# Kernel optimization log

Measured on AMD Instinct MI355X. Metric: run time of the kernel, lower is better.

Reference implementation:

```python
import math
import jax, jax.numpy as jnp
import numpy as np

B, CH3, T = 64, 192, 2048  # B = batch*heads, CH3 = 3*head_dim

def setup_inputs() -> dict:
    key = jax.random.key(0)
    qkv = jax.random.normal(key, (B, CH3, T), dtype=jnp.float32)
    return {"qkv": qkv}

def reference(qkv):
    ch = qkv.shape[1] // 3
    q, k, v = jnp.split(qkv, 3, axis=1)  # each [B, ch, T]
    scale = 1.0 / math.sqrt(math.sqrt(ch))
    # scores [B, T(query), S(key)]
    weight = jnp.einsum('bct,bcs->bts', q * scale, k * scale)
    weight = jax.nn.softmax(weight.astype(jnp.float32), axis=-1).astype(weight.dtype)
    return jnp.einsum('bts,bcs->bct', weight, v)
```

## Files before the change

### kernel.cpp

```cpp
#include <hip/hip_runtime.h>


#define DHEAD 64
#define TLEN  2048
#define NB    64
#define BQ    256
#define BK    64
#define NT    (TLEN / BK)
#define LDT   65

typedef _Float16 h16x8 __attribute__((ext_vector_type(8)));
typedef _Float16 h16x2 __attribute__((ext_vector_type(2)));
typedef __fp16   fp16x2 __attribute__((ext_vector_type(2)));
typedef float    f32x16 __attribute__((ext_vector_type(16)));

#define QK_SCALE 0.42466090267246895f

extern "C" __device__ float __ocml_native_exp2_f32(float);

union H2U  { h16x2 h; fp16x2 f; unsigned u; };
union FRAG { h16x8 v; unsigned u[4]; };

__device__ __forceinline__ unsigned pk_u(float a, float b) {
    H2U x; x.f = __builtin_amdgcn_cvt_pkrtz(a, b); return x.u;
}

__device__ __forceinline__ int swz(int row, int col) {
    return row * 64 + (col ^ ((row & 7) << 3));
}

__global__ __launch_bounds__(256)
void prep_k(const float* __restrict__ qkv, _Float16* __restrict__ ws) {
    __shared__ float T32[64 * LDT];
    const int tile = blockIdx.x, b = blockIdx.y;
    const int tid = threadIdx.x;
    const float* src = qkv + ((size_t)b * 3 + 1) * DHEAD * TLEN + tile * 64;
    _Float16* dst = ws + (size_t)b * DHEAD * TLEN + (size_t)tile * 64 * DHEAD;
    {
        int c = tid >> 4, t4 = (tid & 15) * 4;
        #pragma unroll
        for (int rr = 0; rr < 4; ++rr, c += 16) {
            float4 f = *(const float4*)(src + c * TLEN + t4);
            T32[(t4 + 0) * LDT + c] = f.x;
            T32[(t4 + 1) * LDT + c] = f.y;
            T32[(t4 + 2) * LDT + c] = f.z;
            T32[(t4 + 3) * LDT + c] = f.w;
        }
    }
    __syncthreads();
    #pragma unroll
    for (int rep = 0; rep < 2; ++rep) {
        int idx = rep * 256 + tid;
        int t = idx >> 3, j = idx & 7;
        const float* row = &T32[t * LDT + j * 8];
        FRAG o;
        o.u[0] = pk_u(row[0] * QK_SCALE, row[1] * QK_SCALE);
        o.u[1] = pk_u(row[2] * QK_SCALE, row[3] * QK_SCALE);
        o.u[2] = pk_u(row[4] * QK_SCALE, row[5] * QK_SCALE);
        o.u[3] = pk_u(row[6] * QK_SCALE, row[7] * QK_SCALE);
        *(h16x8*)(dst + t * DHEAD + j * 8) = o.v;
    }
}

__global__ __launch_bounds__(256, 2)
void attn(const float* __restrict__ qkv, const _Float16* __restrict__ kt,
          float* __restrict__ out) {
    __shared__ alignas(16) _Float16 Ks[64 * 64];
    __shared__ alignas(16) _Float16 Vs[64 * 64];

    const int tid  = threadIdx.x;
    const int wave = tid >> 6;
    const int lane = tid & 63;
    const int h    = lane >> 5;
    const int c32  = lane & 31;

    const int flat = blockIdx.x + (int)gridDim.x * blockIdx.y;
    const int j8   = flat & 7, m8 = flat >> 3;
    const int b    = ((m8 & 7) << 3) | j8;
    const int t0   = (m8 >> 3) * BQ + wave * 64;

    const float* qg = qkv + ((size_t)b * 3 + 0) * DHEAD * TLEN;
    const float* vg = qkv + ((size_t)b * 3 + 2) * DHEAD * TLEN;
    const _Float16* kb = kt + (size_t)b * DHEAD * TLEN;

    h16x8 qf[2][4];
    #pragma unroll
    for (int nb = 0; nb < 2; ++nb)
        #pragma unroll
        for (int kbq = 0; kbq < 4; ++kbq) {
            const float* qp = qg + (size_t)(kbq * 16 + h * 8) * TLEN + t0 + nb * 32 + c32;
            FRAG f;
            #pragma unroll
            for (int w = 0; w < 4; ++w)
                f.u[w] = pk_u(qp[(size_t)(2 * w) * TLEN] * QK_SCALE,
                              qp[(size_t)(2 * w + 1) * TLEN] * QK_SCALE);
            qf[nb][kbq] = f.v;
        }

    f32x16 acco[2][2];
    #pragma unroll
    for (int cb = 0; cb < 2; ++cb)
        #pragma unroll
        for (int nb = 0; nb < 2; ++nb)
            #pragma unroll
            for (int r = 0; r < 16; ++r) acco[cb][nb][r] = 0.f;
    float lp[2] = {0.f, 0.f};

    const int sr = tid >> 2;
    const int sq = (tid & 3) * 16;

    h16x8 kc2[2], vc2[2];

    auto PREF = [&](int s0) {
        const _Float16* kp = kb + (size_t)(s0 + sr) * DHEAD + sq;
        kc2[0] = *(const h16x8*)(kp);
        kc2[1] = *(const h16x8*)(kp + 8);
        const float* vp = vg + (size_t)sr * TLEN + s0 + sq;
        float4 v0 = *(const float4*)(vp + 0);
        float4 v1 = *(const float4*)(vp + 4);
        float4 v2 = *(const float4*)(vp + 8);
        float4 v3 = *(const float4*)(vp + 12);
        FRAG a, c;
        a.u[0] = pk_u(v0.x, v0.y); a.u[1] = pk_u(v0.z, v0.w);
        a.u[2] = pk_u(v1.x, v1.y); a.u[3] = pk_u(v1.z, v1.w);
        c.u[0] = pk_u(v2.x, v2.y); c.u[1] = pk_u(v2.z, v2.w);
        c.u[2] = pk_u(v3.x, v3.y); c.u[3] = pk_u(v3.z, v3.w);
        vc2[0] = a.v; vc2[1] = c.v;
    };

    PREF(0);

    for (int it = 0; it < NT; ++it) {
        __syncthreads();
        *(h16x8*)&Ks[swz(sr, sq)]     = kc2[0];
        *(h16x8*)&Ks[swz(sr, sq + 8)] = kc2[1];
        *(h16x8*)&Vs[swz(sr, sq)]     = vc2[0];
        *(h16x8*)&Vs[swz(sr, sq + 8)] = vc2[1];
        __syncthreads();

        if (it + 1 < NT) PREF((it + 1) * BK);

        #pragma unroll
        for (int mb = 0; mb < 2; ++mb) {
            f32x16 accs[2];
            #pragma unroll
            for (int nb = 0; nb < 2; ++nb)
                #pragma unroll
                for (int r = 0; r < 16; ++r) accs[nb][r] = 0.f;

            __builtin_amdgcn_s_setprio(1);
            #pragma unroll
            for (int kbq = 0; kbq < 4; ++kbq) {
                h16x8 ka = *(const h16x8*)&Ks[swz(mb * 32 + c32, kbq * 16 + h * 8)];
                accs[0] = __builtin_amdgcn_mfma_f32_32x32x16_f16(ka, qf[0][kbq], accs[0], 0, 0, 0);
                accs[1] = __builtin_amdgcn_mfma_f32_32x32x16_f16(ka, qf[1][kbq], accs[1], 0, 0, 0);
            }
            __builtin_amdgcn_s_setprio(0);

            h16x8 pb[2][2];
            #pragma unroll
            for (int nb = 0; nb < 2; ++nb) {
                float e[16];
                #pragma unroll
                for (int r = 0; r < 16; ++r) e[r] = __ocml_native_exp2_f32(accs[nb][r]);
                float s0 = 0.f;
                #pragma unroll
                for (int r = 0; r < 16; ++r) s0 += e[r];
                lp[nb] += s0;
                #pragma unroll
                for (int kb16 = 0; kb16 < 2; ++kb16) {
                    const float* ee = e + kb16 * 8;
                    unsigned a01 = pk_u(ee[0], ee[1]);
                    unsigned a23 = pk_u(ee[2], ee[3]);
                    unsigned b01 = pk_u(ee[4], ee[5]);
                    unsigned b23 = pk_u(ee[6], ee[7]);
                    asm volatile("v_permlane32_swap_b32 %0, %1" : "+v"(a01), "+v"(b01));
                    asm volatile("v_permlane32_swap_b32 %0, %1" : "+v"(a23), "+v"(b23));
                    FRAG f;
                    f.u[0] = a01; f.u[1] = a23; f.u[2] = b01; f.u[3] = b23;
                    pb[kb16][nb] = f.v;
                }
            }

            __builtin_amdgcn_s_setprio(1);
            #pragma unroll
            for (int kb16 = 0; kb16 < 2; ++kb16) {
                const int scol = mb * 32 + kb16 * 16 + h * 8;
                #pragma unroll
                for (int cb = 0; cb < 2; ++cb) {
                    h16x8 va = *(const h16x8*)&Vs[swz(cb * 32 + c32, scol)];
                    acco[cb][0] = __builtin_amdgcn_mfma_f32_32x32x16_f16(va, pb[kb16][0], acco[cb][0], 0, 0, 0);
                    acco[cb][1] = __builtin_amdgcn_mfma_f32_32x32x16_f16(va, pb[kb16][1], acco[cb][1], 0, 0, 0);
                }
            }
            __builtin_amdgcn_s_setprio(0);
        }
    }

    float rinv[2];
    #pragma unroll
    for (int nb = 0; nb < 2; ++nb) {
        float l = lp[nb];
        l += __shfl_xor(l, 32);
        rinv[nb] = 1.0f / l;
    }

    float* ob = out + (size_t)b * DHEAD * TLEN + t0;
    #pragma unroll
    for (int cb = 0; cb < 2; ++cb)
        #pragma unroll
        for (int nb = 0; nb < 2; ++nb)
            #pragma unroll
            for (int r = 0; r < 16; ++r) {
                const int c = cb * 32 + (r & 3) + 8 * (r >> 2) + 4 * h;
                ob[(size_t)c * TLEN + nb * 32 + c32] = acco[cb][nb][r] * rinv[nb];
            }
}

extern "C" void kernel_launch(void* const* d_in, const int* in_sizes, int n_in,
                              void* d_out, int out_size, void* d_ws, size_t ws_size,
                              hipStream_t stream) {
    const float* qkv = (const float*)d_in[0];
    _Float16* ws = (_Float16*)d_ws;
    float* out = (float*)d_out;
    prep_k<<<dim3(TLEN / 64, NB), 256, 0, stream>>>(qkv, ws);
    attn<<<dim3(TLEN / BQ, NB), 256, 0, stream>>>(qkv, ws, out);
}
```

Measured before the change: 219.9 us.

## Halve query tile per wave, double-buffer K/V LDS, raise occupancy

Each wave now handles 32 queries instead of 64, so the per-block query tile drops to 128 and the grid doubles. Accumulator and Q-fragment registers are halved, and launch bounds now ask for 4 blocks per CU. K/V shared tiles are double-buffered, which removes one barrier per iteration. The cost is that each K/V tile is reused by half as many queries, doubling global and LDS traffic for K/V per unit of work, and the block-to-(batch, tile) mapping is reworked.

```diff
diff --git a/kernel.cpp b/kernel.cpp
--- a/kernel.cpp
+++ b/kernel.cpp
@@ -4,7 +4,7 @@
 #define DHEAD 64
 #define TLEN  2048
 #define NB    64
-#define BQ    256
+#define BQ    128
 #define BK    64
 #define NT    (TLEN / BK)
 #define LDT   65
@@ -62,11 +62,11 @@
     }
 }
 
-__global__ __launch_bounds__(256, 2)
+__global__ __launch_bounds__(256, 4)
 void attn(const float* __restrict__ qkv, const _Float16* __restrict__ kt,
           float* __restrict__ out) {
-    __shared__ alignas(16) _Float16 Ks[64 * 64];
-    __shared__ alignas(16) _Float16 Vs[64 * 64];
+    __shared__ alignas(16) _Float16 Ks[2][64 * 64];
+    __shared__ alignas(16) _Float16 Vs[2][64 * 64];
 
     const int tid  = threadIdx.x;
     const int wave = tid >> 6;
@@ -75,36 +75,31 @@
     const int c32  = lane & 31;
 
     const int flat = blockIdx.x + (int)gridDim.x * blockIdx.y;
-    const int j8   = flat & 7, m8 = flat >> 3;
-    const int b    = ((m8 & 7) << 3) | j8;
-    const int t0   = (m8 >> 3) * BQ + wave * 64;
+    const int b    = (((flat >> 7) & 7) << 3) | (flat & 7);
+    const int t0   = ((flat >> 3) & 15) * BQ + wave * 32;
 
     const float* qg = qkv + ((size_t)b * 3 + 0) * DHEAD * TLEN;
     const float* vg = qkv + ((size_t)b * 3 + 2) * DHEAD * TLEN;
     const _Float16* kb = kt + (size_t)b * DHEAD * TLEN;
 
-    h16x8 qf[2][4];
-    #pragma unroll
-    for (int nb = 0; nb < 2; ++nb)
-        #pragma unroll
-        for (int kbq = 0; kbq < 4; ++kbq) {
-            const float* qp = qg + (size_t)(kbq * 16 + h * 8) * TLEN + t0 + nb * 32 + c32;
-            FRAG f;
-            #pragma unroll
-            for (int w = 0; w < 4; ++w)
-                f.u[w] = pk_u(qp[(size_t)(2 * w) * TLEN] * QK_SCALE,
-                              qp[(size_t)(2 * w + 1) * TLEN] * QK_SCALE);
-            qf[nb][kbq] = f.v;
-        }
-
-    f32x16 acco[2][2];
+    h16x8 qf[4];
+    #pragma unroll
+    for (int kbq = 0; kbq < 4; ++kbq) {
+        const float* qp = qg + (size_t)(kbq * 16 + h * 8) * TLEN + t0 + c32;
+        FRAG f;
+        #pragma unroll
+        for (int w = 0; w < 4; ++w)
+            f.u[w] = pk_u(qp[(size_t)(2 * w) * TLEN] * QK_SCALE,
+                          qp[(size_t)(2 * w + 1) * TLEN] * QK_SCALE);
+        qf[kbq] = f.v;
+    }
+
+    f32x16 acco[2];
     #pragma unroll
     for (int cb = 0; cb < 2; ++cb)
         #pragma unroll
-        for (int nb = 0; nb < 2; ++nb)
-            #pragma unroll
-            for (int r = 0; r < 16; ++r) acco[cb][nb][r] = 0.f;
-    float lp[2] = {0.f, 0.f};
+        for (int r = 0; r < 16; ++r) acco[cb][r] = 0.f;
+    float lp = 0.f;
 
     const int sr = tid >> 2;
     const int sq = (tid & 3) * 16;
@@ -131,55 +126,51 @@
     PREF(0);
 
     for (int it = 0; it < NT; ++it) {
+        _Float16* ksb = Ks[it & 1];
+        _Float16* vsb = Vs[it & 1];
+        *(h16x8*)&ksb[swz(sr, sq)]     = kc2[0];
+        *(h16x8*)&ksb[swz(sr, sq + 8)] = kc2[1];
+        *(h16x8*)&vsb[swz(sr, sq)]     = vc2[0];
+        *(h16x8*)&vsb[swz(sr, sq + 8)] = vc2[1];
         __syncthreads();
-        *(h16x8*)&Ks[swz(sr, sq)]     = kc2[0];
-        *(h16x8*)&Ks[swz(sr, sq + 8)] = kc2[1];
-        *(h16x8*)&Vs[swz(sr, sq)]     = vc2[0];
-        *(h16x8*)&Vs[swz(sr, sq + 8)] = vc2[1];
-        __syncthreads();
 
         if (it + 1 < NT) PREF((it + 1) * BK);
 
         #pragma unroll
         for (int mb = 0; mb < 2; ++mb) {
-            f32x16 accs[2];
-            #pragma unroll
-            for (int nb = 0; nb < 2; ++nb)
-                #pragma unroll
-                for (int r = 0; r < 16; ++r) accs[nb][r] = 0.f;
+            f32x16 accs;
+            #pragma unroll
+            for (int r = 0; r < 16; ++r) accs[r] = 0.f;
 
             __builtin_amdgcn_s_setprio(1);
             #pragma unroll
             for (int kbq = 0; kbq < 4; ++kbq) {
-                h16x8 ka = *(const h16x8*)&Ks[swz(mb * 32 + c32, kbq * 16 + h * 8)];
-                accs[0] = __builtin_amdgcn_mfma_f32_32x32x16_f16(ka, qf[0][kbq], accs[0], 0, 0, 0);
-                accs[1] = __builtin_amdgcn_mfma_f32_32x32x16_f16(ka, qf[1][kbq], accs[1], 0, 0, 0);
+                h16x8 ka = *(const h16x8*)&ksb[swz(mb * 32 + c32, kbq * 16 + h * 8)];
+                accs = __builtin_amdgcn_mfma_f32_32x32x16_f16(ka, qf[kbq], accs, 0, 0, 0);
             }
             __builtin_amdgcn_s_setprio(0);
 
-            h16x8 pb[2][2];
-            #pragma unroll
-            for (int nb = 0; nb < 2; ++nb) {
-                float e[16];
-                #pragma unroll
-                for (int r = 0; r < 16; ++r) e[r] = __ocml_native_exp2_f32(accs[nb][r]);
-                float s0 = 0.f;
-                #pragma unroll
-                for (int r = 0; r < 16; ++r) s0 += e[r];
-                lp[nb] += s0;
-                #pragma unroll
-                for (int kb16 = 0; kb16 < 2; ++kb16) {
-                    const float* ee = e + kb16 * 8;
-                    unsigned a01 = pk_u(ee[0], ee[1]);
-                    unsigned a23 = pk_u(ee[2], ee[3]);
-                    unsigned b01 = pk_u(ee[4], ee[5]);
-                    unsigned b23 = pk_u(ee[6], ee[7]);
-                    asm volatile("v_permlane32_swap_b32 %0, %1" : "+v"(a01), "+v"(b01));
-                    asm volatile("v_permlane32_swap_b32 %0, %1" : "+v"(a23), "+v"(b23));
-                    FRAG f;
-                    f.u[0] = a01; f.u[1] = a23; f.u[2] = b01; f.u[3] = b23;
-                    pb[kb16][nb] = f.v;
-                }
+            float e[16];
+            #pragma unroll
+            for (int r = 0; r < 16; ++r) e[r] = __ocml_native_exp2_f32(accs[r]);
+            float s0 = 0.f;
+            #pragma unroll
+            for (int r = 0; r < 16; ++r) s0 += e[r];
+            lp += s0;
+
+            h16x8 pb[2];
+            #pragma unroll
+            for (int kb16 = 0; kb16 < 2; ++kb16) {
+                const float* ee = e + kb16 * 8;
+                unsigned a01 = pk_u(ee[0], ee[1]);
+                unsigned a23 = pk_u(ee[2], ee[3]);
+                unsigned b01 = pk_u(ee[4], ee[5]);
+                unsigned b23 = pk_u(ee[6], ee[7]);
+                asm volatile("v_permlane32_swap_b32 %0, %1" : "+v"(a01), "+v"(b01));
+                asm volatile("v_permlane32_swap_b32 %0, %1" : "+v"(a23), "+v"(b23));
+                FRAG f;
+                f.u[0] = a01; f.u[1] = a23; f.u[2] = b01; f.u[3] = b23;
+                pb[kb16] = f.v;
             }
 
             __builtin_amdgcn_s_setprio(1);
@@ -188,33 +179,26 @@
                 const int scol = mb * 32 + kb16 * 16 + h * 8;
                 #pragma unroll
                 for (int cb = 0; cb < 2; ++cb) {
-                    h16x8 va = *(const h16x8*)&Vs[swz(cb * 32 + c32, scol)];
-                    acco[cb][0] = __builtin_amdgcn_mfma_f32_32x32x16_f16(va, pb[kb16][0], acco[cb][0], 0, 0, 0);
-                    acco[cb][1] = __builtin_amdgcn_mfma_f32_32x32x16_f16(va, pb[kb16][1], acco[cb][1], 0, 0, 0);
+                    h16x8 va = *(const h16x8*)&vsb[swz(cb * 32 + c32, scol)];
+                    acco[cb] = __builtin_amdgcn_mfma_f32_32x32x16_f16(va, pb[kb16], acco[cb], 0, 0, 0);
                 }
             }
             __builtin_amdgcn_s_setprio(0);
         }
     }
 
-    float rinv[2];
-    #pragma unroll
-    for (int nb = 0; nb < 2; ++nb) {
-        float l = lp[nb];
-        l += __shfl_xor(l, 32);
-        rinv[nb] = 1.0f / l;
-    }
+    float l = lp;
+    l += __shfl_xor(l, 32);
+    const float rinv = 1.0f / l;
 
     float* ob = out + (size_t)b * DHEAD * TLEN + t0;
     #pragma unroll
     for (int cb = 0; cb < 2; ++cb)
         #pragma unroll
-        for (int nb = 0; nb < 2; ++nb)
-            #pragma unroll
-            for (int r = 0; r < 16; ++r) {
-                const int c = cb * 32 + (r & 3) + 8 * (r >> 2) + 4 * h;
-                ob[(size_t)c * TLEN + nb * 32 + c32] = acco[cb][nb][r] * rinv[nb];
-            }
+        for (int r = 0; r < 16; ++r) {
+            const int c = cb * 32 + (r & 3) + 8 * (r >> 2) + 4 * h;
+            ob[(size_t)c * TLEN + c32] = acco[cb][r] * rinv;
+        }
 }
 
 extern "C" void kernel_launch(void* const* d_in, const int* in_sizes, int n_in,
```

Measured after the change: 228.8 us. +4.1%, slower.

## Split key range across two blocks and add combine kernel

Applied to the files above, without the earlier changes.

Each query tile is now processed by two blocks, each covering half of the key sequence. The grid doubles to 1024 blocks and occupancy is raised to 4 blocks per CU. K fragments are read straight from global memory into registers instead of being staged in LDS. V uses a double-buffered LDS tile with a new layout, which needs only one barrier per iteration. Unnormalised partial outputs and row sums go to workspace, and a third kernel merges and normalises them. This adds extra global traffic and a kernel launch in exchange for more parallelism and less synchronisation.

```diff
diff --git a/kernel.cpp b/kernel.cpp
--- a/kernel.cpp
+++ b/kernel.cpp
@@ -6,8 +6,12 @@
 #define NB    64
 #define BQ    256
 #define BK    64
-#define NT    (TLEN / BK)
+#define HALF_S 1024
+#define NT2   (HALF_S / BK)
 #define LDT   65
+
+#define KT_BYTES (NB * DHEAD * TLEN * 2)
+#define L_BYTES  (2 * NB * TLEN * 4)
 
 typedef _Float16 h16x8 __attribute__((ext_vector_type(8)));
 typedef _Float16 h16x2 __attribute__((ext_vector_type(2)));
@@ -25,8 +29,8 @@
     H2U x; x.f = __builtin_amdgcn_cvt_pkrtz(a, b); return x.u;
 }
 
-__device__ __forceinline__ int swz(int row, int col) {
-    return row * 64 + (col ^ ((row & 7) << 3));
+__device__ __forceinline__ int vidx(int c, int s) {
+    return ((s >> 3) << 9) + (c << 3) + (s & 7);
 }
 
 __global__ __launch_bounds__(256)
@@ -62,11 +66,11 @@
     }
 }
 
-__global__ __launch_bounds__(256, 2)
+__global__ __launch_bounds__(256, 4)
 void attn(const float* __restrict__ qkv, const _Float16* __restrict__ kt,
+          float* __restrict__ lbuf, float* __restrict__ o1,
           float* __restrict__ out) {
-    __shared__ alignas(16) _Float16 Ks[64 * 64];
-    __shared__ alignas(16) _Float16 Vs[64 * 64];
+    __shared__ alignas(16) _Float16 Vs[2][64 * 64];
 
     const int tid  = threadIdx.x;
     const int wave = tid >> 6;
@@ -74,14 +78,18 @@
     const int h    = lane >> 5;
     const int c32  = lane & 31;
 
-    const int flat = blockIdx.x + (int)gridDim.x * blockIdx.y;
-    const int j8   = flat & 7, m8 = flat >> 3;
-    const int b    = ((m8 & 7) << 3) | j8;
-    const int t0   = (m8 >> 3) * BQ + wave * 64;
+    const int flat  = blockIdx.x;
+    const int x     = flat & 7, y = flat >> 3;
+    const int b     = ((y >> 4) << 3) | x;
+    const int inner = y & 15;
+    const int shalf = inner & 1;
+    const int qt    = inner >> 1;
+    const int t0    = qt * BQ + wave * 64;
+    const int sbase = shalf * HALF_S;
 
     const float* qg = qkv + ((size_t)b * 3 + 0) * DHEAD * TLEN;
     const float* vg = qkv + ((size_t)b * 3 + 2) * DHEAD * TLEN;
-    const _Float16* kb = kt + (size_t)b * DHEAD * TLEN;
+    const _Float16* kbp = kt + (size_t)b * DHEAD * TLEN + (size_t)sbase * DHEAD;
 
     h16x8 qf[2][4];
     #pragma unroll
@@ -109,13 +117,9 @@
     const int sr = tid >> 2;
     const int sq = (tid & 3) * 16;
 
-    h16x8 kc2[2], vc2[2];
-
+    h16x8 vc2[2];
     auto PREF = [&](int s0) {
-        const _Float16* kp = kb + (size_t)(s0 + sr) * DHEAD + sq;
-        kc2[0] = *(const h16x8*)(kp);
-        kc2[1] = *(const h16x8*)(kp + 8);
-        const float* vp = vg + (size_t)sr * TLEN + s0 + sq;
+        const float* vp = vg + (size_t)sr * TLEN + sbase + s0 + sq;
         float4 v0 = *(const float4*)(vp + 0);
         float4 v1 = *(const float4*)(vp + 4);
         float4 v2 = *(const float4*)(vp + 8);
@@ -130,15 +134,23 @@
 
     PREF(0);
 
-    for (int it = 0; it < NT; ++it) {
+    for (int it = 0; it < NT2; ++it) {
+        const int s0 = it * BK;
+
+        h16x8 kf[8];
+        #pragma unroll
+        for (int mb = 0; mb < 2; ++mb)
+            #pragma unroll
+            for (int kbq = 0; kbq < 4; ++kbq)
+                kf[mb * 4 + kbq] = *(const h16x8*)(kbp + (size_t)(s0 + mb * 32 + c32) * DHEAD
+                                                   + kbq * 16 + h * 8);
+
+        _Float16* vsb = Vs[it & 1];
+        *(h16x8*)&vsb[vidx(sr, sq)]     = vc2[0];
+        *(h16x8*)&vsb[vidx(sr, sq + 8)] = vc2[1];
         __syncthreads();
-        *(h16x8*)&Ks[swz(sr, sq)]     = kc2[0];
-        *(h16x8*)&Ks[swz(sr, sq + 8)] = kc2[1];
-        *(h16x8*)&Vs[swz(sr, sq)]     = vc2[0];
-        *(h16x8*)&Vs[swz(sr, sq + 8)] = vc2[1];
-        __syncthreads();
-
-        if (it + 1 < NT) PREF((it + 1) * BK);
+
+        if (it + 1 < NT2) PREF((it + 1) * BK);
 
         #pragma unroll
         for (int mb = 0; mb < 2; ++mb) {
@@ -151,7 +163,7 @@
             __builtin_amdgcn_s_setprio(1);
             #pragma unroll
             for (int kbq = 0; kbq < 4; ++kbq) {
-                h16x8 ka = *(const h16x8*)&Ks[swz(mb * 32 + c32, kbq * 16 + h * 8)];
+                h16x8 ka = kf[mb * 4 + kbq];
                 accs[0] = __builtin_amdgcn_mfma_f32_32x32x16_f16(ka, qf[0][kbq], accs[0], 0, 0, 0);
                 accs[1] = __builtin_amdgcn_mfma_f32_32x32x16_f16(ka, qf[1][kbq], accs[1], 0, 0, 0);
             }
@@ -163,10 +175,10 @@
                 float e[16];
                 #pragma unroll
                 for (int r = 0; r < 16; ++r) e[r] = __ocml_native_exp2_f32(accs[nb][r]);
-                float s0 = 0.f;
-                #pragma unroll
-                for (int r = 0; r < 16; ++r) s0 += e[r];
-                lp[nb] += s0;
+                float s0v = 0.f;
+                #pragma unroll
+                for (int r = 0; r < 16; ++r) s0v += e[r];
+                lp[nb] += s0v;
                 #pragma unroll
                 for (int kb16 = 0; kb16 < 2; ++kb16) {
                     const float* ee = e + kb16 * 8;
@@ -188,7 +200,7 @@
                 const int scol = mb * 32 + kb16 * 16 + h * 8;
                 #pragma unroll
                 for (int cb = 0; cb < 2; ++cb) {
-                    h16x8 va = *(const h16x8*)&Vs[swz(cb * 32 + c32, scol)];
+                    h16x8 va = *(const h16x8*)&vsb[vidx(cb * 32 + c32, scol)];
                     acco[cb][0] = __builtin_amdgcn_mfma_f32_32x32x16_f16(va, pb[kb16][0], acco[cb][0], 0, 0, 0);
                     acco[cb][1] = __builtin_amdgcn_mfma_f32_32x32x16_f16(va, pb[kb16][1], acco[cb][1], 0, 0, 0);
                 }
@@ -197,15 +209,15 @@
         }
     }
 
-    float rinv[2];
+    float lsum[2];
     #pragma unroll
     for (int nb = 0; nb < 2; ++nb) {
         float l = lp[nb];
         l += __shfl_xor(l, 32);
-        rinv[nb] = 1.0f / l;
-    }
-
-    float* ob = out + (size_t)b * DHEAD * TLEN + t0;
+        lsum[nb] = l;
+    }
+
+    float* op = (shalf == 0 ? out : o1) + (size_t)b * DHEAD * TLEN + t0;
     #pragma unroll
     for (int cb = 0; cb < 2; ++cb)
         #pragma unroll
@@ -213,16 +225,38 @@
             #pragma unroll
             for (int r = 0; r < 16; ++r) {
                 const int c = cb * 32 + (r & 3) + 8 * (r >> 2) + 4 * h;
-                ob[(size_t)c * TLEN + nb * 32 + c32] = acco[cb][nb][r] * rinv[nb];
-            }
+                op[(size_t)c * TLEN + nb * 32 + c32] = acco[cb][nb][r];
+            }
+    lbuf[(size_t)shalf * NB * TLEN + (size_t)b * TLEN + t0 + lane] = lsum[lane >> 5];
+}
+
+__global__ __launch_bounds__(256)
+void combine(float* __restrict__ out, const float* __restrict__ o1,
+             const float* __restrict__ lbuf) {
+    const size_t i = ((size_t)blockIdx.x * 256 + threadIdx.x) * 4;
+    const int b = (int)(i >> 17);
+    const int t = (int)(i & 2047);
+    float4 a  = *(const float4*)(out + i);
+    float4 c  = *(const float4*)(o1 + i);
+    float4 l0 = *(const float4*)(lbuf + (size_t)b * TLEN + t);
+    float4 l1 = *(const float4*)(lbuf + (size_t)NB * TLEN + (size_t)b * TLEN + t);
+    float4 r;
+    r.x = (a.x + c.x) / (l0.x + l1.x);
+    r.y = (a.y + c.y) / (l0.y + l1.y);
+    r.z = (a.z + c.z) / (l0.z + l1.z);
+    r.w = (a.w + c.w) / (l0.w + l1.w);
+    *(float4*)(out + i) = r;
 }
 
 extern "C" void kernel_launch(void* const* d_in, const int* in_sizes, int n_in,
                               void* d_out, int out_size, void* d_ws, size_t ws_size,
                               hipStream_t stream) {
     const float* qkv = (const float*)d_in[0];
-    _Float16* ws = (_Float16*)d_ws;
     float* out = (float*)d_out;
-    prep_k<<<dim3(TLEN / 64, NB), 256, 0, stream>>>(qkv, ws);
-    attn<<<dim3(TLEN / BQ, NB), 256, 0, stream>>>(qkv, ws, out);
-}
+    _Float16* kt = (_Float16*)d_ws;
+    float* lbuf  = (float*)((char*)d_ws + KT_BYTES);
+    float* o1    = (float*)((char*)d_ws + KT_BYTES + L_BYTES);
+    prep_k<<<dim3(TLEN / 64, NB), 256, 0, stream>>>(qkv, kt);
+    attn<<<dim3(1024), 256, 0, stream>>>(qkv, kt, lbuf, o1, out);
+    combine<<<dim3(NB * DHEAD * TLEN / 1024), 256, 0, stream>>>(out, o1, lbuf);
+}
```

Measured after the change: 445.5 us. 2.03x slower.

## Double-buffer K/V LDS tiles and batch both score blocks before softmax

Applied to the files above, without the earlier changes.

Shared K and V tiles are double-buffered so each iteration needs one barrier instead of two. Within an iteration, both QK^T score blocks are computed first and LDS fragments for K and V are loaded up front, giving the scheduler more independent MFMA and exp work to interleave. The cost is doubled LDS use and more live accumulator registers, which could cause spills or lower occupancy.

```diff
diff --git a/kernel.cpp b/kernel.cpp
--- a/kernel.cpp
+++ b/kernel.cpp
@@ -65,8 +65,8 @@
 __global__ __launch_bounds__(256, 2)
 void attn(const float* __restrict__ qkv, const _Float16* __restrict__ kt,
           float* __restrict__ out) {
-    __shared__ alignas(16) _Float16 Ks[64 * 64];
-    __shared__ alignas(16) _Float16 Vs[64 * 64];
+    __shared__ alignas(16) _Float16 Ks[2][64 * 64];
+    __shared__ alignas(16) _Float16 Vs[2][64 * 64];
 
     const int tid  = threadIdx.x;
     const int wave = tid >> 6;
@@ -131,42 +131,60 @@
     PREF(0);
 
     for (int it = 0; it < NT; ++it) {
+        _Float16* ksb = Ks[it & 1];
+        _Float16* vsb = Vs[it & 1];
+        *(h16x8*)&ksb[swz(sr, sq)]     = kc2[0];
+        *(h16x8*)&ksb[swz(sr, sq + 8)] = kc2[1];
+        *(h16x8*)&vsb[swz(sr, sq)]     = vc2[0];
+        *(h16x8*)&vsb[swz(sr, sq + 8)] = vc2[1];
         __syncthreads();
-        *(h16x8*)&Ks[swz(sr, sq)]     = kc2[0];
-        *(h16x8*)&Ks[swz(sr, sq + 8)] = kc2[1];
-        *(h16x8*)&Vs[swz(sr, sq)]     = vc2[0];
-        *(h16x8*)&Vs[swz(sr, sq + 8)] = vc2[1];
-        __syncthreads();
 
         if (it + 1 < NT) PREF((it + 1) * BK);
 
+        f32x16 accs[2][2];
+        #pragma unroll
+        for (int mb = 0; mb < 2; ++mb)
+            #pragma unroll
+            for (int nb = 0; nb < 2; ++nb)
+                #pragma unroll
+                for (int r = 0; r < 16; ++r) accs[mb][nb][r] = 0.f;
+
         #pragma unroll
         for (int mb = 0; mb < 2; ++mb) {
-            f32x16 accs[2];
-            #pragma unroll
-            for (int nb = 0; nb < 2; ++nb)
-                #pragma unroll
-                for (int r = 0; r < 16; ++r) accs[nb][r] = 0.f;
-
+            h16x8 ka[4];
+            #pragma unroll
+            for (int kbq = 0; kbq < 4; ++kbq)
+                ka[kbq] = *(const h16x8*)&ksb[swz(mb * 32 + c32, kbq * 16 + h * 8)];
             __builtin_amdgcn_s_setprio(1);
             #pragma unroll
             for (int kbq = 0; kbq < 4; ++kbq) {
-                h16x8 ka = *(const h16x8*)&Ks[swz(mb * 32 + c32, kbq * 16 + h * 8)];
-                accs[0] = __builtin_amdgcn_mfma_f32_32x32x16_f16(ka, qf[0][kbq], accs[0], 0, 0, 0);
-                accs[1] = __builtin_amdgcn_mfma_f32_32x32x16_f16(ka, qf[1][kbq], accs[1], 0, 0, 0);
+                accs[mb][0] = __builtin_amdgcn_mfma_f32_32x32x16_f16(ka[kbq], qf[0][kbq], accs[mb][0], 0, 0, 0);
+                accs[mb][1] = __builtin_amdgcn_mfma_f32_32x32x16_f16(ka[kbq], qf[1][kbq], accs[mb][1], 0, 0, 0);
             }
             __builtin_amdgcn_s_setprio(0);
+        }
+
+        #pragma unroll
+        for (int mb = 0; mb < 2; ++mb) {
+            h16x8 va[2][2];
+            #pragma unroll
+            for (int kb16 = 0; kb16 < 2; ++kb16) {
+                const int scol = mb * 32 + kb16 * 16 + h * 8;
+                #pragma unroll
+                for (int cb = 0; cb < 2; ++cb)
+                    va[kb16][cb] = *(const h16x8*)&vsb[swz(cb * 32 + c32, scol)];
+            }
 
             h16x8 pb[2][2];
             #pragma unroll
             for (int nb = 0; nb < 2; ++nb) {
                 float e[16];
                 #pragma unroll
-                for (int r = 0; r < 16; ++r) e[r] = __ocml_native_exp2_f32(accs[nb][r]);
-                float s0 = 0.f;
-                #pragma unroll
-                for (int r = 0; r < 16; ++r) s0 += e[r];
-                lp[nb] += s0;
+                for (int r = 0; r < 16; ++r) e[r] = __ocml_native_exp2_f32(accs[mb][nb][r]);
+                float s0v = 0.f;
+                #pragma unroll
+                for (int r = 0; r < 16; ++r) s0v += e[r];
+                lp[nb] += s0v;
                 #pragma unroll
                 for (int kb16 = 0; kb16 < 2; ++kb16) {
                     const float* ee = e + kb16 * 8;
@@ -184,15 +202,12 @@
 
             __builtin_amdgcn_s_setprio(1);
             #pragma unroll
-            for (int kb16 = 0; kb16 < 2; ++kb16) {
-                const int scol = mb * 32 + kb16 * 16 + h * 8;
+            for (int kb16 = 0; kb16 < 2; ++kb16)
                 #pragma unroll
                 for (int cb = 0; cb < 2; ++cb) {
-                    h16x8 va = *(const h16x8*)&Vs[swz(cb * 32 + c32, scol)];
-                    acco[cb][0] = __builtin_amdgcn_mfma_f32_32x32x16_f16(va, pb[kb16][0], acco[cb][0], 0, 0, 0);
-                    acco[cb][1] = __builtin_amdgcn_mfma_f32_32x32x16_f16(va, pb[kb16][1], acco[cb][1], 0, 0, 0);
+                    acco[cb][0] = __builtin_amdgcn_mfma_f32_32x32x16_f16(va[kb16][cb], pb[kb16][0], acco[cb][0], 0, 0, 0);
+                    acco[cb][1] = __builtin_amdgcn_mfma_f32_32x32x16_f16(va[kb16][cb], pb[kb16][1], acco[cb][1], 0, 0, 0);
                 }
-            }
             __builtin_amdgcn_s_setprio(0);
         }
     }
```

Measured after the change: 218.0 us. Within noise of the previous version (-0.9%).
